# Optimization experiments

Hardware: AMD Instinct MI355X
Metric: run time of the kernel (lower is better)

The kernel has to match this reference:

```python
import jax, jax.numpy as jnp
import numpy as np

N_NODES = 100_000
N_EDGES = 1_600_000
N_GRAPHS = 1_000
VOCAB = 65
D_IN = 128
D_HID = 128


def setup_inputs() -> dict:
    key = jax.random.key(0)
    ks = jax.random.split(key, 12)
    x = jax.random.randint(ks[0], (N_NODES,), 0, VOCAB)
    edge_index = jax.random.randint(ks[1], (2, N_EDGES), 0, N_NODES)
    batch = jnp.sort(jax.random.randint(ks[2], (N_NODES,), 0, N_GRAPHS))

    def lin(k, fan_in, fan_out):
        bound = 1.0 / np.sqrt(fan_in)
        kw, kb = jax.random.split(k)
        W = jax.random.uniform(kw, (fan_in, fan_out), jnp.float32, -bound, bound)
        b = jax.random.uniform(kb, (fan_out,), jnp.float32, -bound, bound)
        return W, b

    emb = jax.random.normal(ks[3], (VOCAB, D_IN), jnp.float32)
    W1, b1 = lin(ks[4], D_IN, D_HID)
    W2, b2 = lin(ks[5], D_HID, D_HID)
    W3, b3 = lin(ks[6], D_HID, D_HID)
    Wf, bf = lin(ks[7], D_HID, 1)
    return {"x": x, "edge_index": edge_index, "batch": batch, "emb": emb,
            "W1": W1, "b1": b1, "W2": W2, "b2": b2, "W3": W3, "b3": b3,
            "Wf": Wf, "bf": bf}


def gcn_conv(h, W, b, src, dst, n):
    # PyG GCNConv: add self-loops, symmetric normalization D^-1/2 A_hat D^-1/2,
    # transform then aggregate messages at dst.
    h = h @ W                                             # [N, H]
    deg = jnp.zeros((n,), h.dtype).at[dst].add(1.0) + 1.0  # self-loop adds 1
    dinv = jax.lax.rsqrt(deg)                             # [N]
    coef = dinv[src] * dinv[dst]                          # [E]
    agg = jax.ops.segment_sum(h[src] * coef[:, None], dst, num_segments=n)
    return agg + h * (dinv * dinv)[:, None] + b           # self-loop term + bias


def reference(x, edge_index, batch, emb, W1, b1, W2, b2, W3, b3, Wf, bf):
    # Embedding with max_norm=1: renormalize looked-up rows to norm <= 1.
    e = emb[x]                                            # [N, D_IN]
    nrm = jnp.linalg.norm(e, axis=-1, keepdims=True)
    e = e * jnp.minimum(1.0, 1.0 / jnp.maximum(nrm, 1e-7))

    src, dst = edge_index[0], edge_index[1]
    h = jax.nn.relu(gcn_conv(e, W1, b1, src, dst, N_NODES))
    h = jax.nn.relu(gcn_conv(h, W2, b2, src, dst, N_NODES))
    h = jax.nn.relu(gcn_conv(h, W3, b3, src, dst, N_NODES))

    g = jax.ops.segment_max(h, batch, num_segments=N_GRAPHS)  # [G, H]
    return (g @ Wf + bf).ravel()                               # [G]
```

## Files before the change

### kernel.cpp

```cpp
#include <hip/hip_runtime.h>
#include <hip/hip_bf16.h>

#define N_NODES  100000
#define N_EDGES  1600000
#define N_GRAPHS 1000
#define D        128
#define CAP      64
#define NBKT     256
#define N_BUCKETS ((N_NODES + NBKT - 1) / NBKT)
#define HWGS     256
#define EPW      ((N_EDGES + HWGS - 1) / HWGS)

typedef __attribute__((ext_vector_type(8))) short bf16x8;
typedef __attribute__((ext_vector_type(4))) float f32x4;

__device__ inline f32x4 mfma16(bf16x8 a, bf16x8 b, f32x4 c) {
    return __builtin_amdgcn_mfma_f32_16x16x32_bf16(a, b, c, 0, 0, 0);
}

__device__ inline unsigned short f2bf(float f) {
    unsigned u = __float_as_uint(f);
    unsigned r = u + 0x7fffu + ((u >> 16) & 1u);
    return (unsigned short)(r >> 16);
}

__global__ __launch_bounds__(256) void k_hist(const int* __restrict__ dst,
                                              int* __restrict__ bcnt,
                                              int* __restrict__ wgoff) {
    __shared__ int hist[N_BUCKETS];
    int t = threadIdx.x, w = blockIdx.x;
    for (int b = t; b < N_BUCKETS; b += 256) hist[b] = 0;
    __syncthreads();
    int e0 = w * EPW, e1 = min(e0 + EPW, N_EDGES);
    for (int i = e0 + t; i < e1; i += 256)
        atomicAdd(&hist[dst[i] >> 8], 1);
    __syncthreads();
    for (int b = t; b < N_BUCKETS; b += 256) {
        int h = hist[b];
        wgoff[w * N_BUCKETS + b] = h ? atomicAdd(&bcnt[b], h) : 0;
    }
}

__global__ __launch_bounds__(512) void k_bscan(const int* __restrict__ bcnt,
                                               int* __restrict__ boff) {
    __shared__ int s[512];
    int t = threadIdx.x;
    int v = (t < N_BUCKETS) ? bcnt[t] : 0;
    s[t] = v;
    __syncthreads();
    for (int off = 1; off < 512; off <<= 1) {
        int val = (t >= off) ? s[t - off] : 0;
        __syncthreads();
        s[t] += val;
        __syncthreads();
    }
    if (t < N_BUCKETS) boff[t] = s[t] - v;
    if (t == 0) boff[N_BUCKETS] = N_EDGES;
}

__global__ __launch_bounds__(256) void k_scat(const int* __restrict__ src,
                                              const int* __restrict__ dst,
                                              const int* __restrict__ boff,
                                              const int* __restrict__ wgoff,
                                              int2* __restrict__ epair) {
    __shared__ int cnt[N_BUCKETS];
    int t = threadIdx.x, w = blockIdx.x;
    for (int b = t; b < N_BUCKETS; b += 256) cnt[b] = 0;
    __syncthreads();
    int e0 = w * EPW, e1 = min(e0 + EPW, N_EDGES);
    for (int i = e0 + t; i < e1; i += 256) {
        int d = dst[i], b = d >> 8;
        int r = atomicAdd(&cnt[b], 1);
        epair[boff[b] + wgoff[w * N_BUCKETS + b] + r] = make_int2(src[i], d);
    }
}

__global__ __launch_bounds__(256) void k_ell(const int2* __restrict__ epair,
                                             const int* __restrict__ boff,
                                             int* __restrict__ ell,
                                             int* __restrict__ fill) {
    __shared__ int cnt_s[NBKT];
    __shared__ int ell_s[NBKT * CAP];
    int t = threadIdx.x, b = blockIdx.x;
    int nb0 = b * NBKT;
    int nn = min(NBKT, N_NODES - nb0);
    for (int i = t; i < NBKT; i += 256) cnt_s[i] = 0;
    __syncthreads();
    int e0 = boff[b], e1 = boff[b + 1];
    for (int i = e0 + t; i < e1; i += 256) {
        int2 e = epair[i];
        int ln = e.y - nb0;
        int r = atomicAdd(&cnt_s[ln], 1);
        if (r < CAP) ell_s[ln * CAP + r] = e.x;
    }
    __syncthreads();
    for (int i = t; i < nn * CAP; i += 256)
        ell[(size_t)nb0 * CAP + i] = ell_s[i];
    if (t < nn) fill[nb0 + t] = cnt_s[t];
}

__global__ __launch_bounds__(256) void k_wprep(const float* __restrict__ W1,
                                               const float* __restrict__ W2,
                                               const float* __restrict__ W3,
                                               short* __restrict__ frag) {
    int L = blockIdx.x;
    const float* W = (L == 0) ? W1 : (L == 1) ? W2 : W3;
    short* fh = frag + (size_t)L * 32768;
    short* fl = fh + 16384;
    int t = threadIdx.x;
    #pragma unroll
    for (int f = 0; f < 8; f++) {
        int id = t + f * 256;
        int lane = id & 63, kb = (id >> 6) & 3, nt = id >> 8;
        int k0 = kb * 32 + (lane >> 4) * 8;
        int n  = nt * 16 + (lane & 15);
        bf16x8 vh, vl;
        #pragma unroll
        for (int j = 0; j < 8; j++) {
            float wv = W[(k0 + j) * 128 + n];
            unsigned short hs = f2bf(wv);
            float hf = __uint_as_float((unsigned)hs << 16);
            vh[j] = (short)hs;
            vl[j] = (short)f2bf(wv - hf);
        }
        *(bf16x8*)&fh[id * 8] = vh;
        *(bf16x8*)&fl[id * 8] = vl;
    }
}

__global__ __launch_bounds__(256) void k_embed(const int* __restrict__ x,
                                               const float* __restrict__ emb,
                                               unsigned short* __restrict__ h) {
    int n = blockIdx.x * 4 + (threadIdx.x >> 6);
    int lane = threadIdx.x & 63;
    if (n >= N_NODES) return;
    int xi = x[n];
    float2 v = ((const float2*)(emb + (size_t)xi * D))[lane];
    float ss = v.x * v.x + v.y * v.y;
    #pragma unroll
    for (int off = 32; off; off >>= 1) ss += __shfl_xor(ss, off);
    float nrm = sqrtf(ss);
    float scale = fminf(1.0f, 1.0f / fmaxf(nrm, 1e-7f));
    unsigned pk = (unsigned)f2bf(v.x * scale) | ((unsigned)f2bf(v.y * scale) << 16);
    ((unsigned*)(h + (size_t)n * D))[lane] = pk;
}

__global__ __launch_bounds__(256) void k_gemm(const unsigned short* __restrict__ A,
                                              const short* __restrict__ frag,
                                              const int* __restrict__ fill,
                                              unsigned short* __restrict__ Cb) {
    __shared__ short Bfrag[2 * 16384];
    int t = threadIdx.x;
    {
        const int4* g4 = (const int4*)frag;
        int4* l4 = (int4*)Bfrag;
        #pragma unroll
        for (int i = 0; i < 16; i++) l4[t + i * 256] = g4[t + i * 256];
    }
    __syncthreads();
    const short* Bh = Bfrag;
    const short* Bl = Bfrag + 16384;

    int w = t >> 6, lane = t & 63;
    int quad = lane >> 4, col = lane & 15;
    size_t r0 = (size_t)blockIdx.x * 128 + w * 32;
    f32x4 acc[2][8];
    #pragma unroll
    for (int r = 0; r < 2; r++)
        #pragma unroll
        for (int n = 0; n < 8; n++) acc[r][n] = (f32x4){0.f, 0.f, 0.f, 0.f};

    #pragma unroll
    for (int kb = 0; kb < 4; kb++) {
        bf16x8 a0 = *(const bf16x8*)&A[(r0 + col)      * D + kb * 32 + quad * 8];
        bf16x8 a1 = *(const bf16x8*)&A[(r0 + 16 + col) * D + kb * 32 + quad * 8];
        #pragma unroll
        for (int nt = 0; nt < 8; nt++) {
            bf16x8 bh = *(const bf16x8*)&Bh[((nt * 4 + kb) * 64 + lane) * 8];
            bf16x8 bl = *(const bf16x8*)&Bl[((nt * 4 + kb) * 64 + lane) * 8];
            acc[0][nt] = mfma16(a0, bh, acc[0][nt]);
            acc[0][nt] = mfma16(a0, bl, acc[0][nt]);
            acc[1][nt] = mfma16(a1, bh, acc[1][nt]);
            acc[1][nt] = mfma16(a1, bl, acc[1][nt]);
        }
    }
    #pragma unroll
    for (int r = 0; r < 2; r++) {
        size_t row = r0 + r * 16 + quad * 4;
        #pragma unroll
        for (int g = 0; g < 4; g++) {
            float dv = (row + g < N_NODES)
                         ? 1.0f / sqrtf((float)fill[row + g] + 1.0f) : 0.f;
            #pragma unroll
            for (int nt = 0; nt < 8; nt++)
                Cb[(row + g) * D + nt * 16 + col] = f2bf(acc[r][nt][g] * dv);
        }
    }
}

__device__ inline void acc8(float* acc, int4 r) {
    unsigned u0 = (unsigned)r.x, u1 = (unsigned)r.y,
             u2 = (unsigned)r.z, u3 = (unsigned)r.w;
    acc[0] += __uint_as_float(u0 << 16);
    acc[1] += __uint_as_float(u0 & 0xffff0000u);
    acc[2] += __uint_as_float(u1 << 16);
    acc[3] += __uint_as_float(u1 & 0xffff0000u);
    acc[4] += __uint_as_float(u2 << 16);
    acc[5] += __uint_as_float(u2 & 0xffff0000u);
    acc[6] += __uint_as_float(u3 << 16);
    acc[7] += __uint_as_float(u3 & 0xffff0000u);
}

template<int BF16OUT>
__global__ __launch_bounds__(256) void k_agg(const unsigned short* __restrict__ hw2,
                                             void* __restrict__ hout,
                                             const int* __restrict__ fill,
                                             const int* __restrict__ ell,
                                             const float* __restrict__ bias) {
    int n = blockIdx.x * 4 + (threadIdx.x >> 6);
    int lane = threadIdx.x & 63;
    if (n >= N_NODES) return;
    int quad = lane >> 4;
    int l16  = lane & 15;
    unsigned cOff = (unsigned)(l16 << 3);
    int fr   = __builtin_amdgcn_readfirstlane(fill[n]);
    int cnt  = min(fr, CAP);

    float acc[8];
    #pragma unroll
    for (int c = 0; c < 8; c++) acc[c] = 0.f;

    int s_l = (lane < cnt) ? ell[(size_t)n * CAP + lane] : N_NODES;

    int iters = (cnt + 15) >> 4;
    int4 Ra[4], Rb[4];
    #pragma unroll
    for (int k = 0; k < 4; k++) {
        int s = __shfl(s_l, k * 4 + quad);
        Ra[k] = *(const int4*)&hw2[((unsigned)s << 7) + cOff];
    }
    for (int it = 1; it < iters; it++) {
        #pragma unroll
        for (int k = 0; k < 4; k++) {
            int s = __shfl(s_l, it * 16 + k * 4 + quad);
            Rb[k] = *(const int4*)&hw2[((unsigned)s << 7) + cOff];
        }
        #pragma unroll
        for (int k = 0; k < 4; k++) acc8(acc, Ra[k]);
        #pragma unroll
        for (int k = 0; k < 4; k++) Ra[k] = Rb[k];
    }
    #pragma unroll
    for (int k = 0; k < 4; k++) acc8(acc, Ra[k]);

    #pragma unroll
    for (int c = 0; c < 8; c++) {
        acc[c] += __shfl_xor(acc[c], 16);
        acc[c] += __shfl_xor(acc[c], 32);
    }
    if (quad == 0) {
        int4 sr = *(const int4*)&hw2[((unsigned)n << 7) + cOff];
        acc8(acc, sr);
        float di = 1.0f / sqrtf((float)fr + 1.0f);
        float4 bA = *(const float4*)&bias[l16 * 8];
        float4 bB = *(const float4*)&bias[l16 * 8 + 4];
        float o[8];
        o[0] = fmaxf(acc[0] * di + bA.x, 0.f);
        o[1] = fmaxf(acc[1] * di + bA.y, 0.f);
        o[2] = fmaxf(acc[2] * di + bA.z, 0.f);
        o[3] = fmaxf(acc[3] * di + bA.w, 0.f);
        o[4] = fmaxf(acc[4] * di + bB.x, 0.f);
        o[5] = fmaxf(acc[5] * di + bB.y, 0.f);
        o[6] = fmaxf(acc[6] * di + bB.z, 0.f);
        o[7] = fmaxf(acc[7] * di + bB.w, 0.f);
        if (BF16OUT) {
            int4 pk;
            pk.x = (int)((unsigned)f2bf(o[0]) | ((unsigned)f2bf(o[1]) << 16));
            pk.y = (int)((unsigned)f2bf(o[2]) | ((unsigned)f2bf(o[3]) << 16));
            pk.z = (int)((unsigned)f2bf(o[4]) | ((unsigned)f2bf(o[5]) << 16));
            pk.w = (int)((unsigned)f2bf(o[6]) | ((unsigned)f2bf(o[7]) << 16));
            *(int4*)&((unsigned short*)hout)[((unsigned)n << 7) + cOff] = pk;
        } else {
            float* orow = (float*)hout + ((size_t)n << 7) + cOff;
            *(float4*)orow       = make_float4(o[0], o[1], o[2], o[3]);
            *(float4*)(orow + 4) = make_float4(o[4], o[5], o[6], o[7]);
        }
    }
}

__global__ void k_bounds(const int* __restrict__ batch, int* __restrict__ gstart,
                         int* __restrict__ gend) {
    int i = blockIdx.x * 256 + threadIdx.x;
    if (i < N_NODES) {
        int b = batch[i];
        atomicMin(&gstart[b], i);
        atomicMax(&gend[b], i + 1);
    }
}

__global__ __launch_bounds__(256) void k_pool(const float* __restrict__ h,
                                              const int* __restrict__ gstart,
                                              const int* __restrict__ gend,
                                              const float* __restrict__ Wf,
                                              const float* __restrict__ bf,
                                              float* __restrict__ out) {
    __shared__ float2 sm[4][64];
    int g = blockIdx.x;
    int w = threadIdx.x >> 6, lane = threadIdx.x & 63;
    int s = gstart[g], e = gend[g];
    float2 m = make_float2(-3.402823466e38f, -3.402823466e38f);
    for (int i = s + w; i < e; i += 4) {
        float2 v = ((const float2*)(h + (size_t)i * D))[lane];
        m.x = fmaxf(m.x, v.x);
        m.y = fmaxf(m.y, v.y);
    }
    sm[w][lane] = m;
    __syncthreads();
    if (w == 0) {
        float2 a = sm[0][lane], b2 = sm[1][lane], c = sm[2][lane], d = sm[3][lane];
        m.x = fmaxf(fmaxf(a.x, b2.x), fmaxf(c.x, d.x));
        m.y = fmaxf(fmaxf(a.y, b2.y), fmaxf(c.y, d.y));
        float2 wf = ((const float2*)Wf)[lane];
        float val = m.x * wf.x + m.y * wf.y;
        #pragma unroll
        for (int off = 32; off; off >>= 1) val += __shfl_xor(val, off);
        if (lane == 0) out[g] = val + bf[0];
    }
}

extern "C" void kernel_launch(void* const* d_in, const int* in_sizes, int n_in,
                              void* d_out, int out_size, void* d_ws, size_t ws_size,
                              hipStream_t stream) {
    const int*   x    = (const int*)d_in[0];
    const int*   ei   = (const int*)d_in[1];
    const int*   batch= (const int*)d_in[2];
    const float* emb  = (const float*)d_in[3];
    const float* W1   = (const float*)d_in[4];
    const float* b1   = (const float*)d_in[5];
    const float* W2   = (const float*)d_in[6];
    const float* b2   = (const float*)d_in[7];
    const float* W3   = (const float*)d_in[8];
    const float* b3   = (const float*)d_in[9];
    const float* Wf   = (const float*)d_in[10];
    const float* bf   = (const float*)d_in[11];
    float* out = (float*)d_out;

    const int* src = ei;
    const int* dst = ei + N_EDGES;

    char* p = (char*)d_ws;
    float*          hA   = (float*)p;          p += (size_t)(N_NODES + 128) * D * 4;
    unsigned short* hAb  = (unsigned short*)hA;
    unsigned short* hwb  = (unsigned short*)p; p += (size_t)(N_NODES + 128) * D * 2;
    int2*           epair= (int2*)hwb;
    int*   fill     = (int*)p;              p += (size_t)N_NODES * 4;
    int*   gend     = (int*)p;              p += (size_t)N_GRAPHS * 4;
    int*   gstart   = (int*)p;              p += (size_t)N_GRAPHS * 4;
    int*   ell      = (int*)p;              p += (size_t)N_NODES * CAP * 4;
    int*   wgoff    = (int*)p;              p += (size_t)HWGS * N_BUCKETS * 4;
    int*   bcnt     = (int*)p;              p += (size_t)(N_BUCKETS + 4) * 4;
    int*   boff     = (int*)p;              p += (size_t)(N_BUCKETS + 4) * 4;
    short* wfrag    = (short*)p;            p += (size_t)3 * 32768 * 2;
    (void)p;

    hipMemsetAsync(bcnt, 0, (size_t)N_BUCKETS * 4, stream);
    hipMemsetAsync(gend, 0, (size_t)N_GRAPHS * 4, stream);
    hipMemsetAsync(gstart, 0x7f, (size_t)N_GRAPHS * 4, stream);

    const int NB = (N_NODES + 255) / 256;
    const int NW = (N_NODES + 3) / 4;
    const int GB = (N_NODES + 127) / 128;

    k_hist <<<HWGS, 256, 0, stream>>>(dst, bcnt, wgoff);
    k_bscan<<<1, 512, 0, stream>>>(bcnt, boff);
    k_scat <<<HWGS, 256, 0, stream>>>(src, dst, boff, wgoff, epair);
    k_ell  <<<N_BUCKETS, 256, 0, stream>>>(epair, boff, ell, fill);

    k_wprep<<<3, 256, 0, stream>>>(W1, W2, W3, wfrag);
    k_embed<<<NW, 256, 0, stream>>>(x, emb, hAb);

    k_gemm  <<<GB, 256, 0, stream>>>(hAb, wfrag,             fill, hwb);
    k_agg<1><<<NW, 256, 0, stream>>>(hwb, hAb, fill, ell, b1);
    k_gemm  <<<GB, 256, 0, stream>>>(hAb, wfrag + 32768,     fill, hwb);
    k_agg<1><<<NW, 256, 0, stream>>>(hwb, hAb, fill, ell, b2);
    k_gemm  <<<GB, 256, 0, stream>>>(hAb, wfrag + 65536,     fill, hwb);
    k_agg<0><<<NW, 256, 0, stream>>>(hwb, hA, fill, ell, b3);

    k_bounds<<<NB, 256, 0, stream>>>(batch, gstart, gend);
    k_pool  <<<N_GRAPHS, 256, 0, stream>>>(hA, gstart, gend, Wf, bf, out);
}
```

Before: 450.2 us.

## Process two nodes per wavefront in aggregation and fuse graph bounds into embed

The aggregation kernel now assigns two destination nodes to each wavefront and interleaves their gathers in a fixed, unrolled schedule capped at four 16-neighbour groups. This raises memory-level parallelism and halves the number of blocks. The separate atomic graph-bounds kernel is removed and its work moved into the embedding kernel, which detects segment boundaries in the sorted batch array with plain stores. The fixed schedule assumes CAP of 64 and N_NODES divisible by 8, and it uses more registers per thread, which may lower occupancy.

```diff
diff --git a/kernel.cpp b/kernel.cpp
--- a/kernel.cpp
+++ b/kernel.cpp
@@ -130,7 +130,16 @@
 
 __global__ __launch_bounds__(256) void k_embed(const int* __restrict__ x,
                                                const float* __restrict__ emb,
-                                               unsigned short* __restrict__ h) {
+                                               unsigned short* __restrict__ h,
+                                               const int* __restrict__ batch,
+                                               int* __restrict__ gstart,
+                                               int* __restrict__ gend) {
+    int gid = blockIdx.x * 256 + threadIdx.x;
+    if (gid < N_NODES) {
+        int b = batch[gid];
+        if (gid == 0 || batch[gid - 1] != b) gstart[b] = gid;
+        if (gid == N_NODES - 1 || batch[gid + 1] != b) gend[b] = gid + 1;
+    }
     int n = blockIdx.x * 4 + (threadIdx.x >> 6);
     int lane = threadIdx.x & 63;
     if (n >= N_NODES) return;
@@ -211,54 +220,79 @@
     acc[7] += __uint_as_float(u3 & 0xffff0000u);
 }
 
+#define LOADGRP(R, S, IT)                                                    \
+    {                                                                        \
+        _Pragma("unroll")                                                    \
+        for (int k = 0; k < 4; k++) {                                        \
+            int s = __shfl((S), (IT) * 16 + k * 4 + quad);                   \
+            R[k] = *(const int4*)&hw2[((unsigned)s << 7) + cOff];            \
+        }                                                                    \
+    }
+#define ACCGRP(A, R)                                                         \
+    {                                                                        \
+        _Pragma("unroll")                                                    \
+        for (int k = 0; k < 4; k++) acc8((A), R[k]);                         \
+    }
+
 template<int BF16OUT>
 __global__ __launch_bounds__(256) void k_agg(const unsigned short* __restrict__ hw2,
                                              void* __restrict__ hout,
                                              const int* __restrict__ fill,
                                              const int* __restrict__ ell,
                                              const float* __restrict__ bias) {
-    int n = blockIdx.x * 4 + (threadIdx.x >> 6);
-    int lane = threadIdx.x & 63;
-    if (n >= N_NODES) return;
+    int w = threadIdx.x >> 6, lane = threadIdx.x & 63;
+    int na = blockIdx.x * 8 + w * 2;
+    int nb = na + 1;
+    if (na >= N_NODES) return;
     int quad = lane >> 4;
     int l16  = lane & 15;
     unsigned cOff = (unsigned)(l16 << 3);
-    int fr   = __builtin_amdgcn_readfirstlane(fill[n]);
-    int cnt  = min(fr, CAP);
-
-    float acc[8];
-    #pragma unroll
-    for (int c = 0; c < 8; c++) acc[c] = 0.f;
-
-    int s_l = (lane < cnt) ? ell[(size_t)n * CAP + lane] : N_NODES;
-
-    int iters = (cnt + 15) >> 4;
-    int4 Ra[4], Rb[4];
-    #pragma unroll
-    for (int k = 0; k < 4; k++) {
-        int s = __shfl(s_l, k * 4 + quad);
-        Ra[k] = *(const int4*)&hw2[((unsigned)s << 7) + cOff];
-    }
-    for (int it = 1; it < iters; it++) {
-        #pragma unroll
-        for (int k = 0; k < 4; k++) {
-            int s = __shfl(s_l, it * 16 + k * 4 + quad);
-            Rb[k] = *(const int4*)&hw2[((unsigned)s << 7) + cOff];
+
+    int fa = __builtin_amdgcn_readfirstlane(fill[na]);
+    int fb = __builtin_amdgcn_readfirstlane(fill[nb]);
+    int ca = min(fa, CAP), cb = min(fb, CAP);
+    int sa = (lane < ca) ? ell[na * CAP + lane] : N_NODES;
+    int sb = (lane < cb) ? ell[nb * CAP + lane] : N_NODES;
+    int ia = (ca + 15) >> 4; ia += (ia == 0);
+    int ib = (cb + 15) >> 4; ib += (ib == 0);
+
+    float accA[8], accB[8];
+    #pragma unroll
+    for (int c = 0; c < 8; c++) { accA[c] = 0.f; accB[c] = 0.f; }
+
+    int4 A0[4], A1[4], B0[4], B1[4];
+    LOADGRP(A0, sa, 0);
+    LOADGRP(B0, sb, 0);
+    if (1 < ia) LOADGRP(A1, sa, 1);
+    ACCGRP(accA, A0);
+    if (1 < ib) LOADGRP(B1, sb, 1);
+    ACCGRP(accB, B0);
+    if (ia > 1 || ib > 1) {
+        if (2 < ia) LOADGRP(A0, sa, 2);
+        if (1 < ia) ACCGRP(accA, A1);
+        if (2 < ib) LOADGRP(B0, sb, 2);
+        if (1 < ib) ACCGRP(accB, B1);
+        if (ia > 2 || ib > 2) {
+            if (3 < ia) LOADGRP(A1, sa, 3);
+            if (2 < ia) ACCGRP(accA, A0);
+            if (3 < ib) LOADGRP(B1, sb, 3);
+            if (2 < ib) ACCGRP(accB, B0);
+            if (3 < ia) ACCGRP(accA, A1);
+            if (3 < ib) ACCGRP(accB, B1);
         }
-        #pragma unroll
-        for (int k = 0; k < 4; k++) acc8(acc, Ra[k]);
-        #pragma unroll
-        for (int k = 0; k < 4; k++) Ra[k] = Rb[k];
-    }
-    #pragma unroll
-    for (int k = 0; k < 4; k++) acc8(acc, Ra[k]);
+    }
 
     #pragma unroll
     for (int c = 0; c < 8; c++) {
-        acc[c] += __shfl_xor(acc[c], 16);
-        acc[c] += __shfl_xor(acc[c], 32);
-    }
-    if (quad == 0) {
+        accA[c] += __shfl_xor(accA[c], 16);
+        accA[c] += __shfl_xor(accA[c], 32);
+        accB[c] += __shfl_xor(accB[c], 16);
+        accB[c] += __shfl_xor(accB[c], 32);
+    }
+    if (quad < 2) {
+        int   n   = quad ? nb : na;
+        int   fr  = quad ? fb : fa;
+        float* acc = quad ? accB : accA;
         int4 sr = *(const int4*)&hw2[((unsigned)n << 7) + cOff];
         acc8(acc, sr);
         float di = 1.0f / sqrtf((float)fr + 1.0f);
@@ -288,16 +322,6 @@
     }
 }
 
-__global__ void k_bounds(const int* __restrict__ batch, int* __restrict__ gstart,
-                         int* __restrict__ gend) {
-    int i = blockIdx.x * 256 + threadIdx.x;
-    if (i < N_NODES) {
-        int b = batch[i];
-        atomicMin(&gstart[b], i);
-        atomicMax(&gend[b], i + 1);
-    }
-}
-
 __global__ __launch_bounds__(256) void k_pool(const float* __restrict__ h,
                                               const int* __restrict__ gstart,
                                               const int* __restrict__ gend,
@@ -367,9 +391,9 @@
     hipMemsetAsync(gend, 0, (size_t)N_GRAPHS * 4, stream);
     hipMemsetAsync(gstart, 0x7f, (size_t)N_GRAPHS * 4, stream);
 
-    const int NB = (N_NODES + 255) / 256;
     const int NW = (N_NODES + 3) / 4;
     const int GB = (N_NODES + 127) / 128;
+    const int AB = N_NODES / 8;
 
     k_hist <<<HWGS, 256, 0, stream>>>(dst, bcnt, wgoff);
     k_bscan<<<1, 512, 0, stream>>>(bcnt, boff);
@@ -377,15 +401,14 @@
     k_ell  <<<N_BUCKETS, 256, 0, stream>>>(epair, boff, ell, fill);
 
     k_wprep<<<3, 256, 0, stream>>>(W1, W2, W3, wfrag);
-    k_embed<<<NW, 256, 0, stream>>>(x, emb, hAb);
+    k_embed<<<NW, 256, 0, stream>>>(x, emb, hAb, batch, gstart, gend);
 
     k_gemm  <<<GB, 256, 0, stream>>>(hAb, wfrag,             fill, hwb);
-    k_agg<1><<<NW, 256, 0, stream>>>(hwb, hAb, fill, ell, b1);
+    k_agg<1><<<AB, 256, 0, stream>>>(hwb, hAb, fill, ell, b1);
     k_gemm  <<<GB, 256, 0, stream>>>(hAb, wfrag + 32768,     fill, hwb);
-    k_agg<1><<<NW, 256, 0, stream>>>(hwb, hAb, fill, ell, b2);
+    k_agg<1><<<AB, 256, 0, stream>>>(hwb, hAb, fill, ell, b2);
     k_gemm  <<<GB, 256, 0, stream>>>(hAb, wfrag + 65536,     fill, hwb);
-    k_agg<0><<<NW, 256, 0, stream>>>(hwb, hA, fill, ell, b3);
-
-    k_bounds<<<NB, 256, 0, stream>>>(batch, gstart, gend);
+    k_agg<0><<<AB, 256, 0, stream>>>(hwb, hA, fill, ell, b3);
+
     k_pool  <<<N_GRAPHS, 256, 0, stream>>>(hA, gstart, gend, Wf, bf, out);
 }
```

New measurement: 399.6 us. 11.2% less time.
